# Kernel optimization log

Hardware: AMD Instinct MI355X
Metric: run time of the kernel (lower is better)

Reference implementation:

```python
import jax, jax.numpy as jnp
import numpy as np

NEG_SLOPE = 0.2  # PyG GATv2Conv default negative_slope
EPS_BN = 1e-5


def gatv2(x, src, dst, ea, Wl, bl, Wr, br, We, att, bias, heads, C):
    """GATv2Conv (PyG semantics, eval mode / no dropout).
    x: [N, Fin]; src/dst: [Et] (self-loops already appended); ea: [Et, edge_dim].
    Returns (out [N, heads*C], alpha [Et, heads])."""
    N = x.shape[0]
    xl = (x @ Wl + bl).reshape(N, heads, C)   # lin_l -> source features
    xr = (x @ Wr + br).reshape(N, heads, C)   # lin_r -> target features
    e = (ea @ We).reshape(-1, heads, C)       # lin_edge (no bias in PyG)
    m = jax.nn.leaky_relu(xl[src] + xr[dst] + e, NEG_SLOPE)  # [Et, H, C]
    logit = jnp.einsum('ehc,hc->eh', m, att)                  # [Et, H]
    # segment softmax over destination node
    amax = jax.ops.segment_max(logit, dst, num_segments=N)
    expv = jnp.exp(logit - amax[dst])
    denom = jax.ops.segment_sum(expv, dst, num_segments=N)
    alpha = expv / (denom[dst] + 1e-16)
    out = jax.ops.segment_sum(xl[src] * alpha[:, :, None], dst, num_segments=N)
    return out.reshape(N, heads * C) + bias, alpha


def setup_inputs() -> dict:
    key = jax.random.key(0)
    ks = list(jax.random.split(key, 20))
    N, E, H, C = 100000, 1600000, 2, 32
    D = H * C  # 64
    def nrm(i, shape, s=0.1):
        return jax.random.normal(ks[i], shape, jnp.float32) * s
    return {
        'x': jax.random.normal(ks[0], (N, 2), jnp.float32),
        'edge_index': jax.random.randint(ks[1], (2, E), 0, N, dtype=jnp.int32),
        'edge_attr': jax.random.uniform(ks[2], (E, 1), dtype=jnp.float32),
        'Wl1': nrm(3, (2, D)), 'bl1': jnp.zeros((D,), jnp.float32),
        'Wr1': nrm(4, (2, D)), 'br1': jnp.zeros((D,), jnp.float32),
        'We1': nrm(5, (1, D)), 'att1': nrm(6, (H, C)), 'bias1': jnp.zeros((D,), jnp.float32),
        'skip_W': nrm(7, (2, D)), 'skip_b': jnp.zeros((D,), jnp.float32),
        'bn_gamma': jnp.ones((D,), jnp.float32), 'bn_beta': jnp.zeros((D,), jnp.float32),
        'Wl2': nrm(8, (D, C)), 'bl2': jnp.zeros((C,), jnp.float32),
        'Wr2': nrm(9, (D, C)), 'br2': jnp.zeros((C,), jnp.float32),
        'We2': nrm(10, (1, C)), 'att2': nrm(11, (1, C)), 'bias2': jnp.zeros((C,), jnp.float32),
        'Wc1': nrm(12, (C, C)), 'bc1': jnp.zeros((C,), jnp.float32),
        'Wc2': nrm(13, (C, 10)), 'bc2': jnp.zeros((10,), jnp.float32),
        'Wt1': nrm(14, (C, C)), 'bt1': jnp.zeros((C,), jnp.float32),
        'Wt2': nrm(15, (C, 20)), 'bt2': jnp.zeros((20,), jnp.float32),
    }


def reference(x, edge_index, edge_attr, Wl1, bl1, Wr1, br1, We1, att1, bias1,
              skip_W, skip_b, bn_gamma, bn_beta,
              Wl2, bl2, Wr2, br2, We2, att2, bias2,
              Wc1, bc1, Wc2, bc2, Wt1, bt1, Wt2, bt2):
    N = x.shape[0]
    src0, dst0 = edge_index[0], edge_index[1]
    # add_self_loops with fill_value='mean': self-loop attr = mean of incoming edge attrs per node
    loop = jnp.arange(N, dtype=edge_index.dtype)
    deg = jax.ops.segment_sum(jnp.ones(src0.shape, jnp.float32), dst0, num_segments=N)
    loop_attr = jax.ops.segment_sum(edge_attr, dst0, num_segments=N) / jnp.maximum(deg, 1.0)[:, None]
    src = jnp.concatenate([src0, loop])
    dst = jnp.concatenate([dst0, loop])
    ea = jnp.concatenate([edge_attr, loop_attr], axis=0)

    h, _ = gatv2(x, src, dst, ea, Wl1, bl1, Wr1, br1, We1, att1, bias1, heads=2, C=32)
    h = h + x @ skip_W + skip_b
    # BatchNorm1d, training-style batch statistics (deterministic)
    mu = h.mean(0)
    var = h.var(0)
    h = (h - mu) / jnp.sqrt(var + EPS_BN) * bn_gamma + bn_beta
    h = jax.nn.elu(h)
    h, alpha = gatv2(h, src, dst, ea, Wl2, bl2, Wr2, br2, We2, att2, bias2, heads=1, C=32)
    h = jax.nn.elu(h)
    h_type = jax.nn.relu(h @ Wt1 + bt1)
    h_clone = jax.nn.relu(h @ Wc1 + bc1)
    h_type = jax.nn.log_softmax(h_type @ Wt2 + bt2, axis=1)
    h_clone = jax.nn.log_softmax(h_clone @ Wc2 + bc2, axis=1)
    out = jnp.concatenate([h_clone, h_type], axis=1)  # [N, 30]
    return out, alpha
```

## Files before the change

### kernel.cpp

```cpp
#include <hip/hip_runtime.h>
#include <math.h>

#define NEG_SLOPE 0.2f
#define CNT_SHIFT 44
#define EA_SCALE 262144.0f
#define EA_INV (1.0f / 262144.0f)

typedef float f2 __attribute__((ext_vector_type(2)));
__device__ __forceinline__ f2 max2(f2 a, f2 b) { return __builtin_elementwise_max(a, b); }
__device__ __forceinline__ f2 lrelu2(f2 m) { return max2(m, m * NEG_SLOPE); }

__device__ __forceinline__ float lrelu(float x) { return fmaxf(x, NEG_SLOPE * x); }
__device__ __forceinline__ float elu1(float x) { return x > 0.f ? x : __expf(x) - 1.f; }


__global__ void k0p(const int* __restrict__ srcA, const int* __restrict__ dstA,
                    const float* __restrict__ ea, const float* __restrict__ x,
                    const float* __restrict__ Wl, const float* __restrict__ bl,
                    const float* __restrict__ Wr, const float* __restrict__ br,
                    const float* __restrict__ We, const float* __restrict__ att,
                    unsigned long long* __restrict__ packed,
                    unsigned short* __restrict__ rankA,
                    float4* __restrict__ evq, int E) {
    __shared__ float sW[7][64];
    if (threadIdx.x < 64) {
        int d = threadIdx.x;
        sW[0][d] = Wl[d];  sW[1][d] = Wl[64 + d];
        sW[2][d] = We[d];  sW[3][d] = att[d];
        sW[4][d] = Wr[d];  sW[5][d] = Wr[64 + d];
        sW[6][d] = bl[d] + br[d];
    }
    __syncthreads();
    int t = blockIdx.x * blockDim.x + threadIdx.x;
    if (t >= E) return;
    int d = dstA[t], s = srcA[t];
    float eav = ea[t];
    unsigned long long inc = (1ULL << CNT_SHIFT)
                           | (unsigned long long)__float2uint_rn(eav * EA_SCALE);
    unsigned long long old = atomicAdd(&packed[d], inc);
    rankA[t] = (unsigned short)(old >> CNT_SHIFT);

    float2 xs = ((const float2*)x)[s];
    float2 xd = ((const float2*)x)[d];
    float l0 = 0.f, l1 = 0.f;
    #pragma unroll
    for (int c = 0; c < 32; ++c) {
        float m0 = xd.x * sW[4][c] + xd.y * sW[5][c] + sW[6][c]
                 + xs.x * sW[0][c] + xs.y * sW[1][c] + eav * sW[2][c];
        l0 += lrelu(m0) * sW[3][c];
        int c2 = c + 32;
        float m1 = xd.x * sW[4][c2] + xd.y * sW[5][c2] + sW[6][c2]
                 + xs.x * sW[0][c2] + xs.y * sW[1][c2] + eav * sW[2][c2];
        l1 += lrelu(m1) * sW[3][c2];
    }
    evq[t] = make_float4(__expf(l0), __expf(l1), xs.x, xs.y);
}

__global__ void kscanA(const unsigned long long* __restrict__ packed,
                       int* __restrict__ rowstart, int* __restrict__ bsum,
                       int* __restrict__ cntA, float* __restrict__ asumA, int N) {
    __shared__ int sm[256];
    int t = threadIdx.x;
    int i = blockIdx.x * 256 + t;
    int v = 0;
    if (i < N) {
        unsigned long long p = packed[i];
        int c = (int)(p >> CNT_SHIFT);
        cntA[i] = c;
        asumA[i] = (float)(p & ((1ULL << CNT_SHIFT) - 1)) * EA_INV;
        v = c + 1;
    }
    sm[t] = v;
    __syncthreads();
    for (int off = 1; off < 256; off <<= 1) {
        int u = (t >= off) ? sm[t - off] : 0;
        __syncthreads();
        sm[t] += u;
        __syncthreads();
    }
    if (i < N) rowstart[i] = sm[t] - v;
    if (t == 255) bsum[blockIdx.x] = sm[255];
}

__global__ void kscanB(int* __restrict__ bsum, int B) {
    __shared__ int sm[512];
    int t = threadIdx.x;
    int v = (t < B) ? bsum[t] : 0;
    sm[t] = v;
    __syncthreads();
    for (int off = 1; off < 512; off <<= 1) {
        int u = (t >= off) ? sm[t - off] : 0;
        __syncthreads();
        sm[t] += u;
        __syncthreads();
    }
    if (t < B) bsum[t] = sm[t] - v;
}

__global__ void kscanC(int* __restrict__ rowstart, const int* __restrict__ bsum, int N) {
    int i = blockIdx.x * blockDim.x + threadIdx.x;
    if (i < N) rowstart[i] += bsum[i >> 8];
}

__global__ void kscatter(const int* __restrict__ srcA, const int* __restrict__ dstA,
                         const float* __restrict__ ea, const float* __restrict__ x,
                         const float* __restrict__ asumA,
                         const int* __restrict__ cntA, const int* __restrict__ rowstart,
                         const unsigned short* __restrict__ rankA,
                         const float4* __restrict__ evq,
                         const float* __restrict__ Wl, const float* __restrict__ bl,
                         const float* __restrict__ Wr, const float* __restrict__ br,
                         const float* __restrict__ We, const float* __restrict__ att,
                         int2* __restrict__ rec, int* __restrict__ posA, int E, int Et) {
    __shared__ float sW[7][64];
    if (threadIdx.x < 64) {
        int d = threadIdx.x;
        sW[0][d] = Wl[d];  sW[1][d] = Wl[64 + d];
        sW[2][d] = We[d];  sW[3][d] = att[d];
        sW[4][d] = Wr[d];  sW[5][d] = Wr[64 + d];
        sW[6][d] = bl[d] + br[d];
    }
    __syncthreads();
    int t = blockIdx.x * blockDim.x + threadIdx.x;
    if (t >= Et) return;
    if (t < E) {
        int d = dstA[t];
        int r = min((int)rankA[t], cntA[d] - 1);
        int pos = rowstart[d] + r;
        rec[(size_t)pos * 4]     = make_int2(srcA[t], __float_as_int(ea[t]));
        ((float4*)rec)[(size_t)pos * 2 + 1] = evq[t];
        posA[t] = pos;
    } else {
        int d = t - E;
        int cd = cntA[d];
        int pos = rowstart[d] + cd;
        float eav = asumA[d] / fmaxf((float)cd, 1.0f);
        float2 xd = ((const float2*)x)[d];
        float l0 = 0.f, l1 = 0.f;
        #pragma unroll
        for (int c = 0; c < 32; ++c) {
            float m0 = xd.x * (sW[4][c] + sW[0][c]) + xd.y * (sW[5][c] + sW[1][c])
                     + sW[6][c] + eav * sW[2][c];
            l0 += lrelu(m0) * sW[3][c];
            int c2 = c + 32;
            float m1 = xd.x * (sW[4][c2] + sW[0][c2]) + xd.y * (sW[5][c2] + sW[1][c2])
                     + sW[6][c2] + eav * sW[2][c2];
            l1 += lrelu(m1) * sW[3][c2];
        }
        rec[(size_t)pos * 4]     = make_int2(d, __float_as_int(eav));
        ((float4*)rec)[(size_t)pos * 2 + 1] =
            make_float4(__expf(l0), __expf(l1), xd.x, xd.y);
    }
}

__global__ void kL1(const int2* __restrict__ rec,
                    const int* __restrict__ rowst, const int* __restrict__ cntA,
                    float* __restrict__ dstat, int N) {
    int g = threadIdx.x >> 4, l16 = threadIdx.x & 15;
    int n = blockIdx.x * 16 + g;
    if (n >= N) return;
    int start = rowst[n], len = cntA[n] + 1;
    const float4* recq = (const float4*)rec;
    float pd0 = 0.f, pd1 = 0.f, pa0 = 0.f, pa1 = 0.f, pb0 = 0.f, pb1 = 0.f;
    for (int i = l16; i < len; i += 16) {
        float4 q = recq[(size_t)(start + i) * 2 + 1];
        pd0 += q.x;        pd1 += q.y;
        pa0 += q.x * q.z;  pa1 += q.y * q.z;
        pb0 += q.x * q.w;  pb1 += q.y * q.w;
    }
    #pragma unroll
    for (int m = 1; m < 16; m <<= 1) {
        pd0 += __shfl_xor(pd0, m); pd1 += __shfl_xor(pd1, m);
        pa0 += __shfl_xor(pa0, m); pa1 += __shfl_xor(pa1, m);
        pb0 += __shfl_xor(pb0, m); pb1 += __shfl_xor(pb1, m);
    }
    if (l16 == 0) {
        float* ps = &dstat[(size_t)n * 6];
        ps[0] = pd0; ps[1] = pd1;
        ps[2] = pa0; ps[3] = pa1;
        ps[4] = pb0; ps[5] = pb1;
    }
}

__global__ void k3a(const float* __restrict__ x, const float* __restrict__ dstat,
                    const float* __restrict__ Wl, const float* __restrict__ bl,
                    const float* __restrict__ bias1,
                    const float* __restrict__ skW, const float* __restrict__ skb,
                    float* __restrict__ hout, float* __restrict__ partial, int N) {
    __shared__ float sv[256], sq[256];
    size_t total = (size_t)N * 64;
    size_t stride = (size_t)gridDim.x * blockDim.x;
    float s = 0.f, q = 0.f;
    for (size_t idx = (size_t)blockIdx.x * blockDim.x + threadIdx.x; idx < total; idx += stride) {
        int n = (int)(idx >> 6), d = (int)(idx & 63), h2 = d >> 5;
        const float* ps = &dstat[(size_t)n * 6];
        float den = ps[h2], t0 = ps[2 + h2], t1 = ps[4 + h2];
        float agg = t0 * Wl[d] + t1 * Wl[64 + d] + den * bl[d];
        float hv = agg / (den + 1e-16f) + bias1[d]
                 + x[2 * n] * skW[d] + x[2 * n + 1] * skW[64 + d] + skb[d];
        hout[idx] = hv;
        s += hv; q += hv * hv;
    }
    sv[threadIdx.x] = s; sq[threadIdx.x] = q;
    __syncthreads();
    if (threadIdx.x < 64) {
        float a = sv[threadIdx.x] + sv[threadIdx.x + 64] + sv[threadIdx.x + 128] + sv[threadIdx.x + 192];
        float b = sq[threadIdx.x] + sq[threadIdx.x + 64] + sq[threadIdx.x + 128] + sq[threadIdx.x + 192];
        partial[(size_t)blockIdx.x * 128 + threadIdx.x] = a;
        partial[(size_t)blockIdx.x * 128 + 64 + threadIdx.x] = b;
    }
}

__global__ void kred(const float* __restrict__ partial, float* __restrict__ mu,
                     float* __restrict__ rstd, int G, int N) {
    __shared__ float s1[256], s2[256];
    int c = blockIdx.x;
    float a = 0.f, b = 0.f;
    for (int i = threadIdx.x; i < G; i += blockDim.x) {
        a += partial[(size_t)i * 128 + c];
        b += partial[(size_t)i * 128 + 64 + c];
    }
    s1[threadIdx.x] = a; s2[threadIdx.x] = b;
    __syncthreads();
    for (int off = 128; off >= 1; off >>= 1) {
        if (threadIdx.x < off) {
            s1[threadIdx.x] += s1[threadIdx.x + off];
            s2[threadIdx.x] += s2[threadIdx.x + off];
        }
        __syncthreads();
    }
    if (threadIdx.x == 0) {
        float m = s1[0] / (float)N;
        float v = s2[0] / (float)N - m * m;
        mu[c] = m;
        rstd[c] = rsqrtf(v + 1e-5f);
    }
}

__global__ void k3c(const float* __restrict__ h, const float* __restrict__ mu,
                    const float* __restrict__ rstd, const float* __restrict__ gamma,
                    const float* __restrict__ beta,
                    const float* __restrict__ Wl, const float* __restrict__ bl,
                    const float* __restrict__ Wr, const float* __restrict__ br,
                    float* __restrict__ xl2, float* __restrict__ xr2, int N) {
    __shared__ float sh[4][64];
    int w = threadIdx.x >> 6, lane = threadIdx.x & 63;
    int n = blockIdx.x * 4 + w;
    bool valid = (n < N);
    if (valid) {
        float hv = h[(size_t)n * 64 + lane];
        hv = (hv - mu[lane]) * rstd[lane] * gamma[lane] + beta[lane];
        sh[w][lane] = elu1(hv);
    }
    __syncthreads();
    if (!valid) return;
    int c = lane & 31;
    const float* W = (lane < 32) ? Wl : Wr;
    const float* b = (lane < 32) ? bl : br;
    float acc = b[c];
    #pragma unroll
    for (int k = 0; k < 64; ++k) acc += sh[w][k] * W[k * 32 + c];
    ((lane < 32) ? xl2 : xr2)[(size_t)n * 32 + c] = acc;
}

__global__ void __launch_bounds__(256, 4)
kL2(const float* __restrict__ xl2, const float* __restrict__ xr2,
    const int2* __restrict__ rec,
    const int* __restrict__ rowst, const int* __restrict__ cntA,
    const float* __restrict__ We, const float* __restrict__ att,
    float* __restrict__ evS, float* __restrict__ h2,
    float* __restrict__ denom2, int N) {
    int g = blockIdx.x * blockDim.x + threadIdx.x;
    int n = g >> 5;
    if (n >= N) return;
    int lane = g & 31;
    int slot = lane >> 3, cl = lane & 7;
    int c4 = cl * 4;
    float4 t4;
    t4 = *(const float4*)(We + c4);                      f2 weva = {t4.x, t4.y}, wevb = {t4.z, t4.w};
    t4 = *(const float4*)(att + c4);                     f2 atva = {t4.x, t4.y}, atvb = {t4.z, t4.w};
    t4 = *(const float4*)(xr2 + (size_t)n * 32 + c4);    f2 xrva = {t4.x, t4.y}, xrvb = {t4.z, t4.w};
    int start = rowst[n], len = cntA[n] + 1;
    float den = 0.f;
    f2 acca = {0.f, 0.f}, accb = {0.f, 0.f};

    for (int base = 0; base < len; base += 8) {
        int iA = base + slot, iB = base + 4 + slot;
        bool aA = iA < len, aB = iB < len;
        int2 eA = rec[(size_t)(start + (aA ? iA : 0)) * 4];
        int2 eB = rec[(size_t)(start + (aB ? iB : 0)) * 4];
        float4 xA4 = *(const float4*)(xl2 + (size_t)eA.x * 32 + c4);
        float4 xB4 = *(const float4*)(xl2 + (size_t)eB.x * 32 + c4);
        f2 xAa = {xA4.x, xA4.y}, xAb = {xA4.z, xA4.w};
        f2 xBa = {xB4.x, xB4.y}, xBb = {xB4.z, xB4.w};
        float evA = __int_as_float(eA.y), evB = __int_as_float(eB.y);
        f2 mAa = xAa + xrva + evA * weva;
        f2 mAb = xAb + xrvb + evA * wevb;
        f2 mBa = xBa + xrva + evB * weva;
        f2 mBb = xBb + xrvb + evB * wevb;
        f2 psA = lrelu2(mAa) * atva + lrelu2(mAb) * atvb;
        f2 psB = lrelu2(mBa) * atva + lrelu2(mBb) * atvb;
        float pA = psA.x + psA.y;
        float pB = psB.x + psB.y;
        pA += __shfl_xor(pA, 1); pB += __shfl_xor(pB, 1);
        pA += __shfl_xor(pA, 2); pB += __shfl_xor(pB, 2);
        pA += __shfl_xor(pA, 4); pB += __shfl_xor(pB, 4);
        float eevA = aA ? __expf(pA) : 0.f;
        float eevB = aB ? __expf(pB) : 0.f;
        if (cl == 0) {
            if (aA) evS[start + iA] = eevA;
            if (aB) evS[start + iB] = eevB;
        }
        den += eevA + eevB;
        acca += eevA * xAa + eevB * xBa;
        accb += eevA * xAb + eevB * xBb;
    }
    #pragma unroll
    for (int m = 8; m <= 16; m <<= 1) {
        den    += __shfl_xor(den, m);
        acca.x += __shfl_xor(acca.x, m);
        acca.y += __shfl_xor(acca.y, m);
        accb.x += __shfl_xor(accb.x, m);
        accb.y += __shfl_xor(accb.y, m);
    }
    float inv = 1.f / (den + 1e-16f);
    if (slot == 0) {
        float4 o = make_float4(acca.x * inv, acca.y * inv, accb.x * inv, accb.y * inv);
        *(float4*)(h2 + (size_t)n * 32 + c4) = o;
    }
    if (lane == 0) denom2[n] = den;
}

__global__ void k4c(const float* __restrict__ evS, const int* __restrict__ posA,
                    const int* __restrict__ dstA, const int* __restrict__ rowst,
                    const int* __restrict__ cntA, const float* __restrict__ denom,
                    float* __restrict__ alpha, int E, int Et) {
    int t = blockIdx.x * blockDim.x + threadIdx.x;
    if (t >= Et) return;
    float ev, den;
    if (t < E) {
        ev = evS[posA[t]];
        den = denom[dstA[t]];
    } else {
        int d = t - E;
        ev = evS[rowst[d] + cntA[d]];
        den = denom[d];
    }
    alpha[t] = ev / (den + 1e-16f);
}

__global__ void __launch_bounds__(256, 1)
k5(const float* __restrict__ h2, const float* __restrict__ bias2,
   const float* __restrict__ Wt1, const float* __restrict__ bt1,
   const float* __restrict__ Wt2, const float* __restrict__ bt2,
   const float* __restrict__ Wc1, const float* __restrict__ bc1,
   const float* __restrict__ Wc2, const float* __restrict__ bc2,
   float* __restrict__ out, int N) {
    __shared__ float sWt1[1024], sWc1[1024], sWt2[640], sWc2[320];
    __shared__ float sbt1[32], sbc1[32], sbt2[20], sbc2[10], sb2[32];
    for (int i = threadIdx.x; i < 1024; i += blockDim.x) { sWt1[i] = Wt1[i]; sWc1[i] = Wc1[i]; }
    for (int i = threadIdx.x; i < 640; i += blockDim.x) sWt2[i] = Wt2[i];
    for (int i = threadIdx.x; i < 320; i += blockDim.x) sWc2[i] = Wc2[i];
    if (threadIdx.x < 32) { sbt1[threadIdx.x] = bt1[threadIdx.x]; sbc1[threadIdx.x] = bc1[threadIdx.x]; sb2[threadIdx.x] = bias2[threadIdx.x]; }
    if (threadIdx.x < 20) sbt2[threadIdx.x] = bt2[threadIdx.x];
    if (threadIdx.x < 10) sbc2[threadIdx.x] = bc2[threadIdx.x];
    __syncthreads();
    int n = blockIdx.x * blockDim.x + threadIdx.x;
    if (n >= N) return;
    float h[32];
    #pragma unroll
    for (int k = 0; k < 32; ++k) h[k] = elu1(h2[(size_t)n * 32 + k] + sb2[k]);
    float lt[20], lc[10];
    #pragma unroll
    for (int o = 0; o < 20; ++o) lt[o] = sbt2[o];
    #pragma unroll
    for (int o = 0; o < 10; ++o) lc[o] = sbc2[o];
    #pragma unroll
    for (int j = 0; j < 32; ++j) {
        float at = sbt1[j], ac = sbc1[j];
        #pragma unroll
        for (int k = 0; k < 32; ++k) { at += h[k] * sWt1[k * 32 + j]; ac += h[k] * sWc1[k * 32 + j]; }
        float tj = fmaxf(at, 0.f), cj = fmaxf(ac, 0.f);
        #pragma unroll
        for (int o = 0; o < 20; ++o) lt[o] += tj * sWt2[j * 20 + o];
        #pragma unroll
        for (int o = 0; o < 10; ++o) lc[o] += cj * sWc2[j * 10 + o];
    }
    float mt = -1e30f, mc = -1e30f;
    #pragma unroll
    for (int o = 0; o < 20; ++o) mt = fmaxf(mt, lt[o]);
    #pragma unroll
    for (int o = 0; o < 10; ++o) mc = fmaxf(mc, lc[o]);
    float st = 0.f, sc = 0.f;
    #pragma unroll
    for (int o = 0; o < 20; ++o) st += __expf(lt[o] - mt);
    #pragma unroll
    for (int o = 0; o < 10; ++o) sc += __expf(lc[o] - mc);
    float lset = mt + __logf(st);
    float lsec = mc + __logf(sc);
    #pragma unroll
    for (int o = 0; o < 10; ++o) out[(size_t)n * 30 + o] = lc[o] - lsec;
    #pragma unroll
    for (int o = 0; o < 20; ++o) out[(size_t)n * 30 + 10 + o] = lt[o] - lset;
}

extern "C" void kernel_launch(void* const* d_in, const int* in_sizes, int n_in,
                              void* d_out, int out_size, void* d_ws, size_t ws_size,
                              hipStream_t stream) {
    const float* x     = (const float*)d_in[0];
    const int*   ei    = (const int*)d_in[1];
    const float* eattr = (const float*)d_in[2];
    const float* Wl1   = (const float*)d_in[3];
    const float* bl1   = (const float*)d_in[4];
    const float* Wr1   = (const float*)d_in[5];
    const float* br1   = (const float*)d_in[6];
    const float* We1   = (const float*)d_in[7];
    const float* att1  = (const float*)d_in[8];
    const float* bias1 = (const float*)d_in[9];
    const float* skW   = (const float*)d_in[10];
    const float* skb   = (const float*)d_in[11];
    const float* gamma = (const float*)d_in[12];
    const float* beta  = (const float*)d_in[13];
    const float* Wl2   = (const float*)d_in[14];
    const float* bl2   = (const float*)d_in[15];
    const float* Wr2   = (const float*)d_in[16];
    const float* br2   = (const float*)d_in[17];
    const float* We2   = (const float*)d_in[18];
    const float* att2  = (const float*)d_in[19];
    const float* bias2 = (const float*)d_in[20];
    const float* Wc1   = (const float*)d_in[21];
    const float* bc1   = (const float*)d_in[22];
    const float* Wc2   = (const float*)d_in[23];
    const float* bc2   = (const float*)d_in[24];
    const float* Wt1   = (const float*)d_in[25];
    const float* bt1   = (const float*)d_in[26];
    const float* Wt2   = (const float*)d_in[27];
    const float* bt2   = (const float*)d_in[28];

    const int N  = in_sizes[0] / 2;
    const int E  = in_sizes[1] / 2;
    const int Et = E + N;
    const int* srcA = ei;
    const int* dstA = ei + E;
    const int G3 = 1024;
    const int B  = (N + 255) / 256;

    char* p = (char*)d_ws;
    unsigned long long* packed = (unsigned long long*)p; p += (size_t)N * 8;
    int2*  rec    = (int2*)p;  p += (size_t)Et * 32;
    int*   posA   = (int*)p;   p += (size_t)E * 4;
    unsigned short* rankA = (unsigned short*)p; p += (size_t)E * 2;
    size_t hbytes = (size_t)N * 64 * 4;
    size_t ebytes = (size_t)E * 16;
    size_t ovl = hbytes > ebytes ? hbytes : ebytes;
    float4* evq   = (float4*)p;
    float*  hbuf  = (float*)p; p += ovl;
    float* xl2    = (float*)p; p += (size_t)N * 32 * 4;
    float* xr2    = (float*)p; p += (size_t)N * 32 * 4;
    float* evS    = (float*)p; p += (size_t)Et * 4;
    float* dstat  = (float*)p; p += (size_t)N * 6 * 4;
    int*   cntA   = (int*)p;   p += (size_t)N * 4;
    float* asumA  = (float*)p; p += (size_t)N * 4;
    int*   rowst  = (int*)p;   p += (size_t)N * 4;
    int*   bsum   = (int*)p;   p += 512 * 4;
    float* partial= (float*)p; p += (size_t)G3 * 128 * 4;
    float* mu     = (float*)p; p += 64 * 4;
    float* rstd   = (float*)p; p += 64 * 4;
    float* denom2 = (float*)p; p += (size_t)N * 4;
    float* h2     = hbuf;

    float* outMain  = (float*)d_out;
    float* outAlpha = outMain + (size_t)N * 30;

    hipMemsetAsync(packed, 0, (size_t)N * 8, stream);
    k0p<<<(E + 255) / 256, 256, 0, stream>>>(srcA, dstA, eattr, x,
                                             Wl1, bl1, Wr1, br1, We1, att1,
                                             packed, rankA, evq, E);
    kscanA<<<B, 256, 0, stream>>>(packed, rowst, bsum, cntA, asumA, N);
    kscanB<<<1, 512, 0, stream>>>(bsum, B);
    kscanC<<<B, 256, 0, stream>>>(rowst, bsum, N);
    kscatter<<<(Et + 255) / 256, 256, 0, stream>>>(srcA, dstA, eattr, x, asumA, cntA,
                                                   rowst, rankA, evq,
                                                   Wl1, bl1, Wr1, br1, We1, att1,
                                                   rec, posA, E, Et);

    kL1<<<(N + 15) / 16, 256, 0, stream>>>(rec, rowst, cntA, dstat, N);

    k3a<<<G3, 256, 0, stream>>>(x, dstat, Wl1, bl1, bias1, skW, skb, hbuf, partial, N);
    kred<<<64, 256, 0, stream>>>(partial, mu, rstd, G3, N);
    k3c<<<(N + 3) / 4, 256, 0, stream>>>(hbuf, mu, rstd, gamma, beta,
                                         Wl2, bl2, Wr2, br2, xl2, xr2, N);

    kL2<<<((size_t)N * 32 + 255) / 256, 256, 0, stream>>>(xl2, xr2, rec, rowst, cntA,
                                                          We2, att2, evS, h2, denom2, N);
    k4c<<<(Et + 255) / 256, 256, 0, stream>>>(evS, posA, dstA, rowst, cntA, denom2,
                                              outAlpha, E, Et);

    k5<<<(N + 255) / 256, 256, 0, stream>>>(h2, bias2, Wt1, bt1, Wt2, bt2,
                                            Wc1, bc1, Wc2, bc2, outMain, N);
    (void)n_in; (void)out_size; (void)ws_size;
}
```

Measured before the change: 324.9 us.

## Move layer-1 logit compute into scatter and shrink CSR edge record to 16 bytes

The per-edge attention logit for layer 1 is now computed in the scatter kernel instead of the atomic counting kernel. This removes the intermediate evq buffer and its write-then-reread round trip. The CSR edge record shrinks from 32 to 16 bytes: it packs src, edge attr and the two exp-logits, and drops the cached source features. As a result, kL1 must gather x[src] indirectly, and kL2 now reads the compact record. This saves bandwidth at the cost of an extra random gather in kL1.

```diff
diff --git a/kernel.cpp b/kernel.cpp
--- a/kernel.cpp
+++ b/kernel.cpp
@@ -3,6 +3,7 @@
 
 #define NEG_SLOPE 0.2f
 #define CNT_SHIFT 44
+#define LOW_MASK ((1ULL << CNT_SHIFT) - 1)
 #define EA_SCALE 262144.0f
 #define EA_INV (1.0f / 262144.0f)
 
@@ -14,46 +15,16 @@
 __device__ __forceinline__ float elu1(float x) { return x > 0.f ? x : __expf(x) - 1.f; }
 
 
-__global__ void k0p(const int* __restrict__ srcA, const int* __restrict__ dstA,
-                    const float* __restrict__ ea, const float* __restrict__ x,
-                    const float* __restrict__ Wl, const float* __restrict__ bl,
-                    const float* __restrict__ Wr, const float* __restrict__ br,
-                    const float* __restrict__ We, const float* __restrict__ att,
+__global__ void k0p(const int* __restrict__ dst, const float* __restrict__ ea,
                     unsigned long long* __restrict__ packed,
-                    unsigned short* __restrict__ rankA,
-                    float4* __restrict__ evq, int E) {
-    __shared__ float sW[7][64];
-    if (threadIdx.x < 64) {
-        int d = threadIdx.x;
-        sW[0][d] = Wl[d];  sW[1][d] = Wl[64 + d];
-        sW[2][d] = We[d];  sW[3][d] = att[d];
-        sW[4][d] = Wr[d];  sW[5][d] = Wr[64 + d];
-        sW[6][d] = bl[d] + br[d];
-    }
-    __syncthreads();
+                    unsigned short* __restrict__ rankA, int E) {
     int t = blockIdx.x * blockDim.x + threadIdx.x;
     if (t >= E) return;
-    int d = dstA[t], s = srcA[t];
-    float eav = ea[t];
+    int d = dst[t];
     unsigned long long inc = (1ULL << CNT_SHIFT)
-                           | (unsigned long long)__float2uint_rn(eav * EA_SCALE);
+                           | (unsigned long long)__float2uint_rn(ea[t] * EA_SCALE);
     unsigned long long old = atomicAdd(&packed[d], inc);
     rankA[t] = (unsigned short)(old >> CNT_SHIFT);
-
-    float2 xs = ((const float2*)x)[s];
-    float2 xd = ((const float2*)x)[d];
-    float l0 = 0.f, l1 = 0.f;
-    #pragma unroll
-    for (int c = 0; c < 32; ++c) {
-        float m0 = xd.x * sW[4][c] + xd.y * sW[5][c] + sW[6][c]
-                 + xs.x * sW[0][c] + xs.y * sW[1][c] + eav * sW[2][c];
-        l0 += lrelu(m0) * sW[3][c];
-        int c2 = c + 32;
-        float m1 = xd.x * sW[4][c2] + xd.y * sW[5][c2] + sW[6][c2]
-                 + xs.x * sW[0][c2] + xs.y * sW[1][c2] + eav * sW[2][c2];
-        l1 += lrelu(m1) * sW[3][c2];
-    }
-    evq[t] = make_float4(__expf(l0), __expf(l1), xs.x, xs.y);
 }
 
 __global__ void kscanA(const unsigned long long* __restrict__ packed,
@@ -67,7 +38,7 @@
         unsigned long long p = packed[i];
         int c = (int)(p >> CNT_SHIFT);
         cntA[i] = c;
-        asumA[i] = (float)(p & ((1ULL << CNT_SHIFT) - 1)) * EA_INV;
+        asumA[i] = (float)(p & LOW_MASK) * EA_INV;
         v = c + 1;
     }
     sm[t] = v;
@@ -107,11 +78,10 @@
                          const float* __restrict__ asumA,
                          const int* __restrict__ cntA, const int* __restrict__ rowstart,
                          const unsigned short* __restrict__ rankA,
-                         const float4* __restrict__ evq,
                          const float* __restrict__ Wl, const float* __restrict__ bl,
                          const float* __restrict__ Wr, const float* __restrict__ br,
                          const float* __restrict__ We, const float* __restrict__ att,
-                         int2* __restrict__ rec, int* __restrict__ posA, int E, int Et) {
+                         float4* __restrict__ rec, int* __restrict__ posA, int E, int Et) {
     __shared__ float sW[7][64];
     if (threadIdx.x < 64) {
         int d = threadIdx.x;
@@ -123,50 +93,48 @@
     __syncthreads();
     int t = blockIdx.x * blockDim.x + threadIdx.x;
     if (t >= Et) return;
+    int s, d, pos; float eav;
     if (t < E) {
-        int d = dstA[t];
+        d = dstA[t]; s = srcA[t]; eav = ea[t];
         int r = min((int)rankA[t], cntA[d] - 1);
-        int pos = rowstart[d] + r;
-        rec[(size_t)pos * 4]     = make_int2(srcA[t], __float_as_int(ea[t]));
-        ((float4*)rec)[(size_t)pos * 2 + 1] = evq[t];
+        pos = rowstart[d] + r;
         posA[t] = pos;
     } else {
-        int d = t - E;
+        d = t - E; s = d;
         int cd = cntA[d];
-        int pos = rowstart[d] + cd;
-        float eav = asumA[d] / fmaxf((float)cd, 1.0f);
-        float2 xd = ((const float2*)x)[d];
-        float l0 = 0.f, l1 = 0.f;
-        #pragma unroll
-        for (int c = 0; c < 32; ++c) {
-            float m0 = xd.x * (sW[4][c] + sW[0][c]) + xd.y * (sW[5][c] + sW[1][c])
-                     + sW[6][c] + eav * sW[2][c];
-            l0 += lrelu(m0) * sW[3][c];
-            int c2 = c + 32;
-            float m1 = xd.x * (sW[4][c2] + sW[0][c2]) + xd.y * (sW[5][c2] + sW[1][c2])
-                     + sW[6][c2] + eav * sW[2][c2];
-            l1 += lrelu(m1) * sW[3][c2];
-        }
-        rec[(size_t)pos * 4]     = make_int2(d, __float_as_int(eav));
-        ((float4*)rec)[(size_t)pos * 2 + 1] =
-            make_float4(__expf(l0), __expf(l1), xd.x, xd.y);
-    }
-}
-
-__global__ void kL1(const int2* __restrict__ rec,
+        pos = rowstart[d] + cd;
+        eav = asumA[d] / fmaxf((float)cd, 1.0f);
+    }
+    float2 xs = ((const float2*)x)[s];
+    float2 xd = ((const float2*)x)[d];
+    float l0 = 0.f, l1 = 0.f;
+    #pragma unroll
+    for (int c = 0; c < 32; ++c) {
+        float m0 = xd.x * sW[4][c] + xd.y * sW[5][c] + sW[6][c]
+                 + xs.x * sW[0][c] + xs.y * sW[1][c] + eav * sW[2][c];
+        l0 += lrelu(m0) * sW[3][c];
+        int c2 = c + 32;
+        float m1 = xd.x * sW[4][c2] + xd.y * sW[5][c2] + sW[6][c2]
+                 + xs.x * sW[0][c2] + xs.y * sW[1][c2] + eav * sW[2][c2];
+        l1 += lrelu(m1) * sW[3][c2];
+    }
+    rec[pos] = make_float4(__int_as_float(s), eav, __expf(l0), __expf(l1));
+}
+
+__global__ void kL1(const float4* __restrict__ rec, const float* __restrict__ x,
                     const int* __restrict__ rowst, const int* __restrict__ cntA,
                     float* __restrict__ dstat, int N) {
     int g = threadIdx.x >> 4, l16 = threadIdx.x & 15;
     int n = blockIdx.x * 16 + g;
     if (n >= N) return;
     int start = rowst[n], len = cntA[n] + 1;
-    const float4* recq = (const float4*)rec;
     float pd0 = 0.f, pd1 = 0.f, pa0 = 0.f, pa1 = 0.f, pb0 = 0.f, pb1 = 0.f;
     for (int i = l16; i < len; i += 16) {
-        float4 q = recq[(size_t)(start + i) * 2 + 1];
-        pd0 += q.x;        pd1 += q.y;
-        pa0 += q.x * q.z;  pa1 += q.y * q.z;
-        pb0 += q.x * q.w;  pb1 += q.y * q.w;
+        float4 q = rec[start + i];
+        float2 xs = ((const float2*)x)[__float_as_int(q.x)];
+        pd0 += q.z;        pd1 += q.w;
+        pa0 += q.z * xs.x; pa1 += q.w * xs.x;
+        pb0 += q.z * xs.y; pb1 += q.w * xs.y;
     }
     #pragma unroll
     for (int m = 1; m < 16; m <<= 1) {
@@ -265,7 +233,7 @@
 
 __global__ void __launch_bounds__(256, 4)
 kL2(const float* __restrict__ xl2, const float* __restrict__ xr2,
-    const int2* __restrict__ rec,
+    const float4* __restrict__ rec,
     const int* __restrict__ rowst, const int* __restrict__ cntA,
     const float* __restrict__ We, const float* __restrict__ att,
     float* __restrict__ evS, float* __restrict__ h2,
@@ -287,13 +255,14 @@
     for (int base = 0; base < len; base += 8) {
         int iA = base + slot, iB = base + 4 + slot;
         bool aA = iA < len, aB = iB < len;
-        int2 eA = rec[(size_t)(start + (aA ? iA : 0)) * 4];
-        int2 eB = rec[(size_t)(start + (aB ? iB : 0)) * 4];
-        float4 xA4 = *(const float4*)(xl2 + (size_t)eA.x * 32 + c4);
-        float4 xB4 = *(const float4*)(xl2 + (size_t)eB.x * 32 + c4);
+        float4 qA = rec[start + (aA ? iA : 0)];
+        float4 qB = rec[start + (aB ? iB : 0)];
+        int sA = __float_as_int(qA.x), sB = __float_as_int(qB.x);
+        float4 xA4 = *(const float4*)(xl2 + (size_t)sA * 32 + c4);
+        float4 xB4 = *(const float4*)(xl2 + (size_t)sB * 32 + c4);
         f2 xAa = {xA4.x, xA4.y}, xAb = {xA4.z, xA4.w};
         f2 xBa = {xB4.x, xB4.y}, xBb = {xB4.z, xB4.w};
-        float evA = __int_as_float(eA.y), evB = __int_as_float(eB.y);
+        float evA = qA.y, evB = qB.y;
         f2 mAa = xAa + xrva + evA * weva;
         f2 mAb = xAb + xrvb + evA * wevb;
         f2 mBa = xBa + xrva + evB * weva;
@@ -447,14 +416,10 @@
 
     char* p = (char*)d_ws;
     unsigned long long* packed = (unsigned long long*)p; p += (size_t)N * 8;
-    int2*  rec    = (int2*)p;  p += (size_t)Et * 32;
+    float4* rec   = (float4*)p; p += (size_t)Et * 16;
     int*   posA   = (int*)p;   p += (size_t)E * 4;
     unsigned short* rankA = (unsigned short*)p; p += (size_t)E * 2;
-    size_t hbytes = (size_t)N * 64 * 4;
-    size_t ebytes = (size_t)E * 16;
-    size_t ovl = hbytes > ebytes ? hbytes : ebytes;
-    float4* evq   = (float4*)p;
-    float*  hbuf  = (float*)p; p += ovl;
+    float* hbuf   = (float*)p; p += (size_t)N * 64 * 4;
     float* xl2    = (float*)p; p += (size_t)N * 32 * 4;
     float* xr2    = (float*)p; p += (size_t)N * 32 * 4;
     float* evS    = (float*)p; p += (size_t)Et * 4;
@@ -473,18 +438,16 @@
     float* outAlpha = outMain + (size_t)N * 30;
 
     hipMemsetAsync(packed, 0, (size_t)N * 8, stream);
-    k0p<<<(E + 255) / 256, 256, 0, stream>>>(srcA, dstA, eattr, x,
-                                             Wl1, bl1, Wr1, br1, We1, att1,
-                                             packed, rankA, evq, E);
+    k0p<<<(E + 255) / 256, 256, 0, stream>>>(dstA, eattr, packed, rankA, E);
     kscanA<<<B, 256, 0, stream>>>(packed, rowst, bsum, cntA, asumA, N);
     kscanB<<<1, 512, 0, stream>>>(bsum, B);
     kscanC<<<B, 256, 0, stream>>>(rowst, bsum, N);
     kscatter<<<(Et + 255) / 256, 256, 0, stream>>>(srcA, dstA, eattr, x, asumA, cntA,
-                                                   rowst, rankA, evq,
+                                                   rowst, rankA,
                                                    Wl1, bl1, Wr1, br1, We1, att1,
                                                    rec, posA, E, Et);
 
-    kL1<<<(N + 15) / 16, 256, 0, stream>>>(rec, rowst, cntA, dstat, N);
+    kL1<<<(N + 15) / 16, 256, 0, stream>>>(rec, x, rowst, cntA, dstat, N);
 
     k3a<<<G3, 256, 0, stream>>>(x, dstat, Wl1, bl1, bias1, skW, skb, hbuf, partial, N);
     kred<<<64, 256, 0, stream>>>(partial, mu, rstd, G3, N);
```

Result: no change. 324.7 us (median of 2 runs) (-0.0%).
